# Performance work log

Hardware: AMD Instinct MI355X
Metric: run time of the kernel (lower is better)

The kernel has to match this reference:

```python
import jax, jax.numpy as jnp
import numpy as np

N = 4096        # nodes
E = 262144      # edges (avg degree 64)
F_IN = 8        # num_features
EMB = 4         # embedding_dim
HEADS = 4
G1 = 64         # GATConv1_dim (concat -> 256)
G2 = 16         # GATConv2_dim (concat -> d_model=64)
D = HEADS * G2  # 64
FF = 32         # ff_hid_dim
GRAPHS = 8
OUT = 4         # output_dim
SLOPE_GAT = 0.2   # PyG GATConv negative_slope
SLOPE = 0.01      # F.leaky_relu default

def _p(k, shape, scale=0.1):
    return jax.random.normal(k, shape, jnp.float32) * scale

def setup_inputs() -> dict:
    key = jax.random.key(0)
    ks = jax.random.split(key, 16)
    return {
        "x": jax.random.normal(ks[0], (N, F_IN), jnp.float32),
        "edge_index": jax.random.randint(ks[1], (2, E), 0, N),
        "batch": jnp.sort(jax.random.randint(ks[2], (N,), 0, GRAPHS)),
        "W_feat": _p(ks[3], (F_IN, EMB)), "b_feat": jnp.zeros((EMB,), jnp.float32),
        "W1": _p(ks[4], (EMB, HEADS * G1)), "as1": _p(ks[5], (HEADS, G1)), "ad1": _p(ks[6], (HEADS, G1)), "b1": jnp.zeros((HEADS * G1,), jnp.float32),
        "W2": _p(ks[7], (HEADS * G1, HEADS * G2)), "as2": _p(ks[8], (HEADS, G2)), "ad2": _p(ks[9], (HEADS, G2)), "b2": jnp.zeros((HEADS * G2,), jnp.float32),
        "enc_W1": _p(ks[10], (D, FF)), "enc_b1": jnp.zeros((FF,), jnp.float32),
        "enc_W2": _p(ks[11], (FF, D)), "enc_b2": jnp.zeros((D,), jnp.float32),
        "dec_W1": _p(ks[12], (D, FF)), "dec_b1": jnp.zeros((FF,), jnp.float32),
        "dec_W2": _p(ks[13], (FF, D)), "dec_b2": jnp.zeros((D,), jnp.float32),
        "W_fc": _p(ks[14], (D, OUT)), "b_fc": jnp.zeros((OUT,), jnp.float32),
    }

def _gat(x, src, dst, W, a_s, a_d, b, n):
    # PyG GATConv: h = W x; e_ij = LeakyReLU(a_src.h_j + a_dst.h_i); softmax over
    # edges grouped by destination i; out_i = sum_j alpha_ij h_j; concat heads + bias.
    h = (x @ W).reshape(n, HEADS, -1)                      # [N,H,C]
    logits = (h * a_s).sum(-1)[src] + (h * a_d).sum(-1)[dst]  # [E,H]
    e = jax.nn.leaky_relu(logits, SLOPE_GAT)
    m = jax.ops.segment_max(e, dst, num_segments=n)        # [N,H]
    ex = jnp.exp(e - m[dst])
    den = jax.ops.segment_sum(ex, dst, num_segments=n)
    alpha = ex / (den[dst] + 1e-16)                        # [E,H]
    out = jax.ops.segment_sum(h[src] * alpha[:, :, None], dst, num_segments=n)
    return out.reshape(n, -1) + b

def reference(x, edge_index, batch, W_feat, b_feat, W1, as1, ad1, b1, W2, as2, ad2, b2, enc_W1, enc_b1, enc_W2, enc_b2, dec_W1, dec_b1, dec_W2, dec_b2, W_fc, b_fc):
    src, dst = edge_index[0], edge_index[1]
    h = x @ W_feat + b_feat                                # feature_fc
    h = jax.nn.leaky_relu(_gat(h, src, dst, W1, as1, ad1, b1, N), SLOPE)
    h = jax.nn.leaky_relu(_gat(h, src, dst, W2, as2, ad2, b2, N), SLOPE)
    # Source bug preserved: encoder/decoder MultiheadAttention outputs are computed
    # and then DISCARDED (FFN reads the layer input), so attention never affects the
    # output and is omitted here (pure dead code). Encoder output `memory` is also
    # unused by the decoder FFN, but is computed for parity.
    memory = jax.nn.relu(jax.nn.relu(h @ enc_W1 + enc_b1) @ enc_W2 + enc_b2)
    t = jax.nn.relu(jax.nn.relu(h @ dec_W1 + dec_b1) @ dec_W2 + dec_b2)
    cnt = jax.ops.segment_sum(jnp.ones((N,), jnp.float32), batch, num_segments=GRAPHS)
    pooled = jax.ops.segment_sum(t, batch, num_segments=GRAPHS) / jnp.maximum(cnt, 1.0)[:, None]
    return pooled @ W_fc + b_fc                            # [GRAPHS, OUT]
```

## Files before the change

kernel.cpp:

```cpp
#include <hip/hip_runtime.h>
#include <math.h>

#define NN 4096
#define EE 262144
#define NCHUNK 64
#define CHSZ 4096
#define PAD 128
#define NGRAPHS 8

__device__ __forceinline__ float lrelu(float x, float s){ return x > 0.f ? x : s*x; }

__global__ __launch_bounds__(256) void k_n1hist(
    const float* __restrict__ x, const float* __restrict__ Wf,
    const float* __restrict__ bf, const float* __restrict__ W1,
    const float* __restrict__ as1, const float* __restrict__ ad1,
    const int* __restrict__ ei,
    float* __restrict__ emb4, float* __restrict__ asum1, float* __restrict__ adsum1,
    int* __restrict__ hist){
  __shared__ int shi[NN];
  int t = threadIdx.x, b = blockIdx.x;
  if (b < NCHUNK){
    for (int v=t; v<NN; v+=256) shi[v]=0;
    __syncthreads();
    int base = b*CHSZ;
    #pragma unroll
    for (int i=0;i<16;i++){
      int d = ei[EE + base + i*256 + t];
      atomicAdd(&shi[d], 1);
    }
    __syncthreads();
    for (int v=t; v<NN; v+=256) hist[b*NN + v] = shi[v];
    return;
  }
  int wid = t >> 6, lane = t & 63;
  int n = (b - NCHUNK)*4 + wid;
  float e0=bf[0], e1=bf[1], e2=bf[2], e3=bf[3];
  #pragma unroll
  for (int k=0;k<8;k++){
    float xv = x[n*8+k];
    e0 += xv*Wf[k*4+0]; e1 += xv*Wf[k*4+1];
    e2 += xv*Wf[k*4+2]; e3 += xv*Wf[k*4+3];
  }
  if (lane == 0) *(float4*)&emb4[n*4] = make_float4(e0,e1,e2,e3);
  int c0 = lane*4;
  float4 w0 = *(const float4*)&W1[0*256+c0];
  float4 w1 = *(const float4*)&W1[1*256+c0];
  float4 w2 = *(const float4*)&W1[2*256+c0];
  float4 w3 = *(const float4*)&W1[3*256+c0];
  float4 hv;
  hv.x = e0*w0.x + e1*w1.x + e2*w2.x + e3*w3.x;
  hv.y = e0*w0.y + e1*w1.y + e2*w2.y + e3*w3.y;
  hv.z = e0*w0.z + e1*w1.z + e2*w2.z + e3*w3.z;
  hv.w = e0*w0.w + e1*w1.w + e2*w2.w + e3*w3.w;
  int hh = lane>>4, idx = c0 & 63;
  float4 as = *(const float4*)&as1[hh*64+idx];
  float4 ad = *(const float4*)&ad1[hh*64+idx];
  float ps = hv.x*as.x + hv.y*as.y + hv.z*as.z + hv.w*as.w;
  float pd = hv.x*ad.x + hv.y*ad.y + hv.z*ad.z + hv.w*ad.w;
  #pragma unroll
  for (int m=1;m<16;m<<=1){ ps += __shfl_xor(ps,m,64); pd += __shfl_xor(pd,m,64); }
  if ((lane&15)==0){ asum1[n*4+hh]=ps; adsum1[n*4+hh]=pd; }
}

__global__ __launch_bounds__(256) void k_colscan(
    const int* __restrict__ hist, int* __restrict__ bases, int* __restrict__ deg){
  __shared__ int tile[64][65];
  int t = threadIdx.x, b = blockIdx.x;
  int v0 = b*64;
  for (int idx=t; idx<64*64; idx+=256){
    int c = idx>>6, v = idx&63;
    tile[c][v] = hist[c*NN + v0 + v];
  }
  __syncthreads();
  if (t < 64){
    int s = 0;
    #pragma unroll
    for (int c=0;c<64;c++){
      int xch = tile[c][t];
      tile[c][t] = (v0+t)*PAD + s;
      s += xch;
    }
    deg[v0+t] = s;
  }
  __syncthreads();
  for (int idx=t; idx<64*64; idx+=256){
    int c = idx>>6, v = idx&63;
    bases[c*NN + v0 + v] = tile[c][v];
  }
}

__global__ __launch_bounds__(256) void k_scatter(
    const int* __restrict__ ei, const int* __restrict__ bases,
    int* __restrict__ esrc){
  __shared__ int shi[NN];
  int t = threadIdx.x, c = blockIdx.x;
  for (int v=t; v<NN; v+=256) shi[v] = bases[c*NN + v];
  __syncthreads();
  int base = c*CHSZ;
  #pragma unroll
  for (int i=0;i<16;i++){
    int e = base + i*256 + t;
    int d = ei[EE+e], sr = ei[e];
    int pos = atomicAdd(&shi[d], 1);
    esrc[pos] = sr;
  }
}

__global__ __launch_bounds__(1024) void k_gat1n2(
    const int* __restrict__ deg, const int* __restrict__ esrc,
    const float* __restrict__ emb4, const float* __restrict__ asum1,
    const float* __restrict__ adsum1, const float* __restrict__ b1,
    const float* __restrict__ W1, const float* __restrict__ W2,
    const float* __restrict__ as2, const float* __restrict__ ad2,
    float* __restrict__ h2, float* __restrict__ asum2, float* __restrict__ adsum2){
  __shared__ __align__(16) float g1s[16*256];
  __shared__ __align__(16) float4 w2t[1024];
  int t = threadIdx.x, w = t>>6, lane = t&63;
  const int n = blockIdx.x*16 + w;
  const int start = n*PAD;
  const int dg = deg[n];
  const int hh = lane>>4;
  float4 adst = *(const float4*)&adsum1[n*4];
  int k0 = lane, k1 = lane+64;
  int j0 = esrc[start + (k0<dg ? k0 : 0)];
  int j1 = esrc[start + (k1<dg ? k1 : 0)];
  float4 a0 = *(const float4*)&asum1[j0*4];
  float4 a1 = *(const float4*)&asum1[j1*4];
  float4 mx;
  mx.x = k0<dg ? a0.x : -INFINITY;  mx.y = k0<dg ? a0.y : -INFINITY;
  mx.z = k0<dg ? a0.z : -INFINITY;  mx.w = k0<dg ? a0.w : -INFINITY;
  if (k1<dg){
    mx.x=fmaxf(mx.x,a1.x); mx.y=fmaxf(mx.y,a1.y);
    mx.z=fmaxf(mx.z,a1.z); mx.w=fmaxf(mx.w,a1.w);
  }
  #pragma unroll
  for (int m=1;m<64;m<<=1){
    mx.x=fmaxf(mx.x,__shfl_xor(mx.x,m,64));
    mx.y=fmaxf(mx.y,__shfl_xor(mx.y,m,64));
    mx.z=fmaxf(mx.z,__shfl_xor(mx.z,m,64));
    mx.w=fmaxf(mx.w,__shfl_xor(mx.w,m,64));
  }
  float4 mh;
  mh.x = lrelu(mx.x+adst.x,0.2f); mh.y = lrelu(mx.y+adst.y,0.2f);
  mh.z = lrelu(mx.z+adst.z,0.2f); mh.w = lrelu(mx.w+adst.w,0.2f);
  float4 ex0 = make_float4(0.f,0.f,0.f,0.f), ex1 = make_float4(0.f,0.f,0.f,0.f);
  if (k0<dg){
    ex0.x = expf(lrelu(a0.x+adst.x,0.2f)-mh.x);
    ex0.y = expf(lrelu(a0.y+adst.y,0.2f)-mh.y);
    ex0.z = expf(lrelu(a0.z+adst.z,0.2f)-mh.z);
    ex0.w = expf(lrelu(a0.w+adst.w,0.2f)-mh.w);
  }
  if (k1<dg){
    ex1.x = expf(lrelu(a1.x+adst.x,0.2f)-mh.x);
    ex1.y = expf(lrelu(a1.y+adst.y,0.2f)-mh.y);
    ex1.z = expf(lrelu(a1.z+adst.z,0.2f)-mh.z);
    ex1.w = expf(lrelu(a1.w+adst.w,0.2f)-mh.w);
  }
  float4 den = make_float4(ex0.x+ex1.x, ex0.y+ex1.y, ex0.z+ex1.z, ex0.w+ex1.w);
  #pragma unroll
  for (int m=1;m<64;m<<=1){
    den.x += __shfl_xor(den.x,m,64); den.y += __shfl_xor(den.y,m,64);
    den.z += __shfl_xor(den.z,m,64); den.w += __shfl_xor(den.w,m,64);
  }
  float4 al0, al1;
  al0.x = ex0.x/(den.x+1e-16f); al0.y = ex0.y/(den.y+1e-16f);
  al0.z = ex0.z/(den.z+1e-16f); al0.w = ex0.w/(den.w+1e-16f);
  al1.x = ex1.x/(den.x+1e-16f); al1.y = ex1.y/(den.y+1e-16f);
  al1.z = ex1.z/(den.z+1e-16f); al1.w = ex1.w/(den.w+1e-16f);
  float4 e0v = *(const float4*)&emb4[j0*4];
  float4 e1v = *(const float4*)&emb4[j1*4];
  float4 s0, s1, s2, s3;
  s0.x = al0.x*e0v.x + al1.x*e1v.x; s0.y = al0.x*e0v.y + al1.x*e1v.y;
  s0.z = al0.x*e0v.z + al1.x*e1v.z; s0.w = al0.x*e0v.w + al1.x*e1v.w;
  s1.x = al0.y*e0v.x + al1.y*e1v.x; s1.y = al0.y*e0v.y + al1.y*e1v.y;
  s1.z = al0.y*e0v.z + al1.y*e1v.z; s1.w = al0.y*e0v.w + al1.y*e1v.w;
  s2.x = al0.z*e0v.x + al1.z*e1v.x; s2.y = al0.z*e0v.y + al1.z*e1v.y;
  s2.z = al0.z*e0v.z + al1.z*e1v.z; s2.w = al0.z*e0v.w + al1.z*e1v.w;
  s3.x = al0.w*e0v.x + al1.w*e1v.x; s3.y = al0.w*e0v.y + al1.w*e1v.y;
  s3.z = al0.w*e0v.z + al1.w*e1v.z; s3.w = al0.w*e0v.w + al1.w*e1v.w;
  #pragma unroll
  for (int m=1;m<64;m<<=1){
    s0.x += __shfl_xor(s0.x,m,64); s0.y += __shfl_xor(s0.y,m,64);
    s0.z += __shfl_xor(s0.z,m,64); s0.w += __shfl_xor(s0.w,m,64);
    s1.x += __shfl_xor(s1.x,m,64); s1.y += __shfl_xor(s1.y,m,64);
    s1.z += __shfl_xor(s1.z,m,64); s1.w += __shfl_xor(s1.w,m,64);
    s2.x += __shfl_xor(s2.x,m,64); s2.y += __shfl_xor(s2.y,m,64);
    s2.z += __shfl_xor(s2.z,m,64); s2.w += __shfl_xor(s2.w,m,64);
    s3.x += __shfl_xor(s3.x,m,64); s3.y += __shfl_xor(s3.y,m,64);
    s3.z += __shfl_xor(s3.z,m,64); s3.w += __shfl_xor(s3.w,m,64);
  }
  float4 sh = (hh==0) ? s0 : (hh==1) ? s1 : (hh==2) ? s2 : s3;
  const int c0 = lane*4;
  float4 w0 = *(const float4*)&W1[0*256+c0];
  float4 w1 = *(const float4*)&W1[1*256+c0];
  float4 w2 = *(const float4*)&W1[2*256+c0];
  float4 w3 = *(const float4*)&W1[3*256+c0];
  float4 bb = *(const float4*)&b1[c0];
  float4 o;
  o.x = lrelu(sh.x*w0.x + sh.y*w1.x + sh.z*w2.x + sh.w*w3.x + bb.x, 0.01f);
  o.y = lrelu(sh.x*w0.y + sh.y*w1.y + sh.z*w2.y + sh.w*w3.y + bb.y, 0.01f);
  o.z = lrelu(sh.x*w0.z + sh.y*w1.z + sh.z*w2.z + sh.w*w3.z + bb.z, 0.01f);
  o.w = lrelu(sh.x*w0.w + sh.y*w1.w + sh.z*w2.w + sh.w*w3.w + bb.w, 0.01f);
  ((float4*)&g1s[w*256])[lane] = o;
  __syncthreads();
  float acc2 = 0.f;
  for (int kt=0; kt<4; kt++){
    w2t[t] = ((const float4*)W2)[kt*1024 + t];
    __syncthreads();
    const float* g1row = &g1s[w*256 + kt*64];
    const float* wt = (const float*)w2t;
    #pragma unroll 8
    for (int k=0;k<64;k++) acc2 += g1row[k] * wt[k*64 + lane];
    __syncthreads();
  }
  h2[n*64+lane] = acc2;
  int idx = lane&15;
  float ps = acc2 * as2[hh*16+idx];
  float pd = acc2 * ad2[hh*16+idx];
  #pragma unroll
  for (int m=1;m<16;m<<=1){ ps += __shfl_xor(ps,m,64); pd += __shfl_xor(pd,m,64); }
  if (idx == 0){ asum2[n*4+hh] = ps; adsum2[n*4+hh] = pd; }
}

__global__ __launch_bounds__(1024) void k_gat2(
    const int* __restrict__ deg, const int* __restrict__ esrc,
    const float* __restrict__ h2, const float* __restrict__ asum2,
    const float* __restrict__ adsum2, const float* __restrict__ b2,
    const float* __restrict__ dW1, const float* __restrict__ db1,
    const float* __restrict__ dW2, const float* __restrict__ db2,
    float* __restrict__ tbuf){
  __shared__ float4 smx[8][2];
  __shared__ float4 sdn[8][2];
  __shared__ __align__(16) float salpha[8*512];
  __shared__ float sacc[8][2][64];
  __shared__ float sg[8][96];
  int t = threadIdx.x, w = t>>6, lane = t&63;
  const int p = w>>1, tw = w&1;
  const int n = blockIdx.x*8 + p;
  const int start = n*PAD;
  const int dg = deg[n];
  const int hh = lane>>4;
  float4 adst = *(const float4*)&adsum2[n*4];
  const int k = tw*64 + lane;
  int j = esrc[start + (k<dg ? k : 0)];
  float4 a = *(const float4*)&asum2[j*4];
  float4 mx;
  mx.x = k<dg ? a.x : -INFINITY;  mx.y = k<dg ? a.y : -INFINITY;
  mx.z = k<dg ? a.z : -INFINITY;  mx.w = k<dg ? a.w : -INFINITY;
  #pragma unroll
  for (int m=1;m<64;m<<=1){
    mx.x=fmaxf(mx.x,__shfl_xor(mx.x,m,64));
    mx.y=fmaxf(mx.y,__shfl_xor(mx.y,m,64));
    mx.z=fmaxf(mx.z,__shfl_xor(mx.z,m,64));
    mx.w=fmaxf(mx.w,__shfl_xor(mx.w,m,64));
  }
  if (lane==0) smx[p][tw] = mx;
  __syncthreads();
  float4 m0 = smx[p][0], m1 = smx[p][1];
  float4 mh;
  mh.x = lrelu(fmaxf(m0.x,m1.x)+adst.x,0.2f);
  mh.y = lrelu(fmaxf(m0.y,m1.y)+adst.y,0.2f);
  mh.z = lrelu(fmaxf(m0.z,m1.z)+adst.z,0.2f);
  mh.w = lrelu(fmaxf(m0.w,m1.w)+adst.w,0.2f);
  float4 ex = make_float4(0.f,0.f,0.f,0.f);
  if (k<dg){
    ex.x = expf(lrelu(a.x+adst.x,0.2f)-mh.x);
    ex.y = expf(lrelu(a.y+adst.y,0.2f)-mh.y);
    ex.z = expf(lrelu(a.z+adst.z,0.2f)-mh.z);
    ex.w = expf(lrelu(a.w+adst.w,0.2f)-mh.w);
  }
  float4 dn = ex;
  #pragma unroll
  for (int m=1;m<64;m<<=1){
    dn.x += __shfl_xor(dn.x,m,64); dn.y += __shfl_xor(dn.y,m,64);
    dn.z += __shfl_xor(dn.z,m,64); dn.w += __shfl_xor(dn.w,m,64);
  }
  if (lane==0) sdn[p][tw] = dn;
  __syncthreads();
  float4 d0 = sdn[p][0], d1 = sdn[p][1];
  float4 inv4 = make_float4(1.f/(d0.x+d1.x+1e-16f), 1.f/(d0.y+d1.y+1e-16f),
                            1.f/(d0.z+d1.z+1e-16f), 1.f/(d0.w+d1.w+1e-16f));
  if (k<dg){
    float4 al = make_float4(ex.x*inv4.x, ex.y*inv4.y, ex.z*inv4.z, ex.w*inv4.w);
    *(float4*)&salpha[p*512 + k*4] = al;
  }
  float acc = 0.f;
  int cnt = dg - tw*64; cnt = cnt < 0 ? 0 : (cnt > 64 ? 64 : cnt);
  #pragma unroll 4
  for (int k2=0; k2<cnt; k2++){
    int jj = esrc[start + tw*64 + k2];
    float al = salpha[p*512 + (tw*64+k2)*4 + hh];
    acc += al * h2[jj*64 + lane];
  }
  sacc[p][tw][lane] = acc;
  __syncthreads();
  if (tw==0){
    float tot = sacc[p][0][lane] + sacc[p][1][lane];
    float g2v = lrelu(tot + b2[lane], 0.01f);
    float* sgp = sg[p];
    sgp[lane] = g2v;
    int m = lane & 31;
    float a2 = db1[m];
    #pragma unroll
    for (int kk=0;kk<64;kk++) a2 += sgp[kk] * dW1[kk*32+m];
    if (lane < 32) sgp[64+m] = fmaxf(a2, 0.f);
    float tv = db2[lane];
    #pragma unroll
    for (int kk=0;kk<32;kk++) tv += sgp[64+kk] * dW2[kk*64+lane];
    tbuf[n*64 + lane] = fmaxf(tv, 0.f);
  }
}

__global__ __launch_bounds__(1024) void k_pool(
    const float* __restrict__ tbuf, const int* __restrict__ batch,
    const float* __restrict__ W_fc, const float* __restrict__ b_fc,
    float* __restrict__ out){
  __shared__ float4 part[64][17];
  int t = threadIdx.x, g = blockIdx.x;
  int rg = t>>4, cg = t&15;
  int lo=0, hi=NN;
  while (lo<hi){ int mid=(lo+hi)>>1; if (batch[mid] < g) lo=mid+1; else hi=mid; }
  int s0 = lo;
  lo=0; hi=NN;
  while (lo<hi){ int mid=(lo+hi)>>1; if (batch[mid] < g+1) lo=mid+1; else hi=mid; }
  int e0 = lo;
  float4 acc = make_float4(0.f,0.f,0.f,0.f);
  #pragma unroll 4
  for (int n=s0+rg; n<e0; n+=64){
    float4 v = *(const float4*)&tbuf[n*64 + cg*4];
    acc.x += v.x; acc.y += v.y; acc.z += v.z; acc.w += v.w;
  }
  part[rg][cg] = acc;
  __syncthreads();
  #pragma unroll
  for (int step=32; step>=1; step>>=1){
    if (rg < step){
      float4 o = part[rg+step][cg], m = part[rg][cg];
      part[rg][cg] = make_float4(m.x+o.x, m.y+o.y, m.z+o.z, m.w+o.w);
    }
    __syncthreads();
  }
  if (t < 16){
    float inv = 1.f/fmaxf((float)(e0-s0), 1.f);
    float4 s = part[0][t];
    float4 pm = make_float4(s.x*inv, s.y*inv, s.z*inv, s.w*inv);
    float4 w0 = *(const float4*)&W_fc[(4*t+0)*4];
    float4 w1 = *(const float4*)&W_fc[(4*t+1)*4];
    float4 w2 = *(const float4*)&W_fc[(4*t+2)*4];
    float4 w3 = *(const float4*)&W_fc[(4*t+3)*4];
    float4 po;
    po.x = pm.x*w0.x + pm.y*w1.x + pm.z*w2.x + pm.w*w3.x;
    po.y = pm.x*w0.y + pm.y*w1.y + pm.z*w2.y + pm.w*w3.y;
    po.z = pm.x*w0.z + pm.y*w1.z + pm.z*w2.z + pm.w*w3.z;
    po.w = pm.x*w0.w + pm.y*w1.w + pm.z*w2.w + pm.w*w3.w;
    #pragma unroll
    for (int m=1;m<16;m<<=1){
      po.x += __shfl_xor(po.x,m,64); po.y += __shfl_xor(po.y,m,64);
      po.z += __shfl_xor(po.z,m,64); po.w += __shfl_xor(po.w,m,64);
    }
    if (t == 0){
      float4 bb = *(const float4*)&b_fc[0];
      *(float4*)&out[g*4] = make_float4(po.x+bb.x, po.y+bb.y, po.z+bb.z, po.w+bb.w);
    }
  }
}

extern "C" void kernel_launch(void* const* d_in, const int* in_sizes, int n_in,
                              void* d_out, int out_size, void* d_ws, size_t ws_size,
                              hipStream_t stream){
  const float* x      = (const float*)d_in[0];
  const int*   ei     = (const int*)  d_in[1];
  const int*   batch  = (const int*)  d_in[2];
  const float* W_feat = (const float*)d_in[3];
  const float* b_feat = (const float*)d_in[4];
  const float* W1     = (const float*)d_in[5];
  const float* as1    = (const float*)d_in[6];
  const float* ad1    = (const float*)d_in[7];
  const float* b1     = (const float*)d_in[8];
  const float* W2     = (const float*)d_in[9];
  const float* as2    = (const float*)d_in[10];
  const float* ad2    = (const float*)d_in[11];
  const float* b2     = (const float*)d_in[12];
  const float* dW1    = (const float*)d_in[17];
  const float* db1    = (const float*)d_in[18];
  const float* dW2    = (const float*)d_in[19];
  const float* db2    = (const float*)d_in[20];
  const float* W_fc   = (const float*)d_in[21];
  const float* b_fc   = (const float*)d_in[22];
  float* out = (float*)d_out;

  char* ws = (char*)d_ws;
  float* h2     = (float*)(ws + 0);
  float* tbuf   = (float*)(ws + 1048576);
  int*   hist   = (int*)  (ws + 2097152);
  int*   bases  = (int*)  (ws + 3145728);
  int*   esrc   = (int*)  (ws + 4194304);
  float* emb4   = (float*)(ws + 6291456);
  float* asum1  = (float*)(ws + 6356992);
  float* adsum1 = (float*)(ws + 6422528);
  float* asum2  = (float*)(ws + 6488064);
  float* adsum2 = (float*)(ws + 6553600);
  int*   deg    = (int*)  (ws + 6619136);

  k_n1hist <<<NCHUNK + NN/4, 256, 0, stream>>>(x, W_feat, b_feat, W1, as1, ad1,
                                               ei, emb4, asum1, adsum1, hist);
  k_colscan<<<NN/64,         256, 0, stream>>>(hist, bases, deg);
  k_scatter<<<NCHUNK,        256, 0, stream>>>(ei, bases, esrc);
  k_gat1n2 <<<NN/16,        1024, 0, stream>>>(deg, esrc, emb4, asum1, adsum1, b1,
                                               W1, W2, as2, ad2, h2, asum2, adsum2);
  k_gat2   <<<NN/8,         1024, 0, stream>>>(deg, esrc, h2, asum2, adsum2, b2,
                                               dW1, db1, dW2, db2, tbuf);
  k_pool   <<<NGRAPHS,      1024, 0, stream>>>(tbuf, batch, W_fc, b_fc, out);
}
```

Baseline: 65.85 us.

## Split GAT2 edge aggregation across four waves per node and precompute graph bounds

The layer-2 GAT kernel now gives each node four 64-lane waves instead of two, splitting the edge aggregation into quarters, and launches twice as many blocks. The aim is more parallelism and shorter per-wave gather loops over neighbor features. Graph start offsets for pooling are now found once in the colscan kernel, replacing the per-thread binary searches in the pool kernel. The cost is idle waves during the softmax phase, an extra barrier, and a four-way partial-sum reduction.

After: 72.00 us. 1.09x slower.

```diff
diff --git a/kernel.cpp b/kernel.cpp
--- a/kernel.cpp
+++ b/kernel.cpp
@@ -63,10 +63,17 @@
 }
 
 __global__ __launch_bounds__(256) void k_colscan(
-    const int* __restrict__ hist, int* __restrict__ bases, int* __restrict__ deg){
+    const int* __restrict__ hist, const int* __restrict__ batch,
+    int* __restrict__ bases, int* __restrict__ deg, int* __restrict__ gstart){
   __shared__ int tile[64][65];
   int t = threadIdx.x, b = blockIdx.x;
   int v0 = b*64;
+  if (b == 0 && t >= 64 && t < 64 + NGRAPHS + 1){
+    int g = t - 64;
+    int lo=0, hi=NN;
+    while (lo<hi){ int mid=(lo+hi)>>1; if (batch[mid] < g) lo=mid+1; else hi=mid; }
+    gstart[g]=lo;
+  }
   for (int idx=t; idx<64*64; idx+=256){
     int c = idx>>6, v = idx&63;
     tile[c][v] = hist[c*NN + v0 + v];
@@ -229,24 +236,29 @@
     const float* __restrict__ dW1, const float* __restrict__ db1,
     const float* __restrict__ dW2, const float* __restrict__ db2,
     float* __restrict__ tbuf){
-  __shared__ float4 smx[8][2];
-  __shared__ float4 sdn[8][2];
-  __shared__ __align__(16) float salpha[8*512];
-  __shared__ float sacc[8][2][64];
-  __shared__ float sg[8][96];
+  __shared__ float4 smx[4][2];
+  __shared__ float4 sdn[4][2];
+  __shared__ __align__(16) float salpha[4*512];
+  __shared__ float sacc[4][4][64];
+  __shared__ float sg[4][96];
   int t = threadIdx.x, w = t>>6, lane = t&63;
-  const int p = w>>1, tw = w&1;
-  const int n = blockIdx.x*8 + p;
+  const int p = w>>2, tw = w&3;
+  const int n = blockIdx.x*4 + p;
   const int start = n*PAD;
   const int dg = deg[n];
   const int hh = lane>>4;
   float4 adst = *(const float4*)&adsum2[n*4];
   const int k = tw*64 + lane;
-  int j = esrc[start + (k<dg ? k : 0)];
-  float4 a = *(const float4*)&asum2[j*4];
+  float4 a = make_float4(0.f,0.f,0.f,0.f);
+  int j = 0;
+  if (tw < 2){
+    j = esrc[start + (k<dg ? k : 0)];
+    a = *(const float4*)&asum2[j*4];
+  }
   float4 mx;
-  mx.x = k<dg ? a.x : -INFINITY;  mx.y = k<dg ? a.y : -INFINITY;
-  mx.z = k<dg ? a.z : -INFINITY;  mx.w = k<dg ? a.w : -INFINITY;
+  bool live = (tw<2) && (k<dg);
+  mx.x = live ? a.x : -INFINITY;  mx.y = live ? a.y : -INFINITY;
+  mx.z = live ? a.z : -INFINITY;  mx.w = live ? a.w : -INFINITY;
   #pragma unroll
   for (int m=1;m<64;m<<=1){
     mx.x=fmaxf(mx.x,__shfl_xor(mx.x,m,64));
@@ -254,7 +266,7 @@
     mx.z=fmaxf(mx.z,__shfl_xor(mx.z,m,64));
     mx.w=fmaxf(mx.w,__shfl_xor(mx.w,m,64));
   }
-  if (lane==0) smx[p][tw] = mx;
+  if (tw < 2 && lane==0) smx[p][tw] = mx;
   __syncthreads();
   float4 m0 = smx[p][0], m1 = smx[p][1];
   float4 mh;
@@ -263,7 +275,7 @@
   mh.z = lrelu(fmaxf(m0.z,m1.z)+adst.z,0.2f);
   mh.w = lrelu(fmaxf(m0.w,m1.w)+adst.w,0.2f);
   float4 ex = make_float4(0.f,0.f,0.f,0.f);
-  if (k<dg){
+  if (live){
     ex.x = expf(lrelu(a.x+adst.x,0.2f)-mh.x);
     ex.y = expf(lrelu(a.y+adst.y,0.2f)-mh.y);
     ex.z = expf(lrelu(a.z+adst.z,0.2f)-mh.z);
@@ -275,27 +287,29 @@
     dn.x += __shfl_xor(dn.x,m,64); dn.y += __shfl_xor(dn.y,m,64);
     dn.z += __shfl_xor(dn.z,m,64); dn.w += __shfl_xor(dn.w,m,64);
   }
-  if (lane==0) sdn[p][tw] = dn;
+  if (tw < 2 && lane==0) sdn[p][tw] = dn;
   __syncthreads();
   float4 d0 = sdn[p][0], d1 = sdn[p][1];
   float4 inv4 = make_float4(1.f/(d0.x+d1.x+1e-16f), 1.f/(d0.y+d1.y+1e-16f),
                             1.f/(d0.z+d1.z+1e-16f), 1.f/(d0.w+d1.w+1e-16f));
-  if (k<dg){
+  if (live){
     float4 al = make_float4(ex.x*inv4.x, ex.y*inv4.y, ex.z*inv4.z, ex.w*inv4.w);
     *(float4*)&salpha[p*512 + k*4] = al;
   }
+  __syncthreads();
   float acc = 0.f;
-  int cnt = dg - tw*64; cnt = cnt < 0 ? 0 : (cnt > 64 ? 64 : cnt);
+  int c0e = (dg*tw)>>2, c1e = (dg*(tw+1))>>2;
   #pragma unroll 4
-  for (int k2=0; k2<cnt; k2++){
-    int jj = esrc[start + tw*64 + k2];
-    float al = salpha[p*512 + (tw*64+k2)*4 + hh];
+  for (int k2=c0e; k2<c1e; k2++){
+    int jj = esrc[start + k2];
+    float al = salpha[p*512 + k2*4 + hh];
     acc += al * h2[jj*64 + lane];
   }
   sacc[p][tw][lane] = acc;
   __syncthreads();
   if (tw==0){
-    float tot = sacc[p][0][lane] + sacc[p][1][lane];
+    float tot = sacc[p][0][lane] + sacc[p][1][lane]
+              + sacc[p][2][lane] + sacc[p][3][lane];
     float g2v = lrelu(tot + b2[lane], 0.01f);
     float* sgp = sg[p];
     sgp[lane] = g2v;
@@ -312,18 +326,13 @@
 }
 
 __global__ __launch_bounds__(1024) void k_pool(
-    const float* __restrict__ tbuf, const int* __restrict__ batch,
+    const float* __restrict__ tbuf, const int* __restrict__ gstart,
     const float* __restrict__ W_fc, const float* __restrict__ b_fc,
     float* __restrict__ out){
   __shared__ float4 part[64][17];
   int t = threadIdx.x, g = blockIdx.x;
   int rg = t>>4, cg = t&15;
-  int lo=0, hi=NN;
-  while (lo<hi){ int mid=(lo+hi)>>1; if (batch[mid] < g) lo=mid+1; else hi=mid; }
-  int s0 = lo;
-  lo=0; hi=NN;
-  while (lo<hi){ int mid=(lo+hi)>>1; if (batch[mid] < g+1) lo=mid+1; else hi=mid; }
-  int e0 = lo;
+  int s0 = gstart[g], e0 = gstart[g+1];
   float4 acc = make_float4(0.f,0.f,0.f,0.f);
   #pragma unroll 4
   for (int n=s0+rg; n<e0; n+=64){
@@ -401,14 +410,15 @@
   float* asum2  = (float*)(ws + 6488064);
   float* adsum2 = (float*)(ws + 6553600);
   int*   deg    = (int*)  (ws + 6619136);
+  int*   gstart = (int*)  (ws + 6635520);
 
   k_n1hist <<<NCHUNK + NN/4, 256, 0, stream>>>(x, W_feat, b_feat, W1, as1, ad1,
                                                ei, emb4, asum1, adsum1, hist);
-  k_colscan<<<NN/64,         256, 0, stream>>>(hist, bases, deg);
+  k_colscan<<<NN/64,         256, 0, stream>>>(hist, batch, bases, deg, gstart);
   k_scatter<<<NCHUNK,        256, 0, stream>>>(ei, bases, esrc);
   k_gat1n2 <<<NN/16,        1024, 0, stream>>>(deg, esrc, emb4, asum1, adsum1, b1,
                                                W1, W2, as2, ad2, h2, asum2, adsum2);
-  k_gat2   <<<NN/8,         1024, 0, stream>>>(deg, esrc, h2, asum2, adsum2, b2,
+  k_gat2   <<<NN/4,         1024, 0, stream>>>(deg, esrc, h2, asum2, adsum2, b2,
                                                dW1, db1, dW2, db2, tbuf);
-  k_pool   <<<NGRAPHS,      1024, 0, stream>>>(tbuf, batch, W_fc, b_fc, out);
-}
+  k_pool   <<<NGRAPHS,      1024, 0, stream>>>(tbuf, gstart, W_fc, b_fc, out);
+}
```
